# Optimization experiments

Hardware: AMD Instinct MI355X
Metric: run time of the kernel (lower is better)

## Reference

```python
import math
import jax, jax.numpy as jnp
import numpy as np

BATCH, DEPTH = 16, 12
N_NODES = 2 ** DEPTH - 1  # 4095, heap layout: children of i are 2i+1, 2i+2
IN_F, OUT_F, STATE_F = 512, 512, 256


def setup_inputs() -> dict:
    key = jax.random.key(0)
    ks = jax.random.split(key, 10)
    x_batch = jax.random.normal(ks[0], (BATCH, N_NODES, IN_F), dtype=jnp.float32)
    idx_batch = jnp.arange(BATCH, dtype=jnp.int32)
    W_in = jax.random.normal(ks[1], (IN_F, IN_F), dtype=jnp.float32) / math.sqrt(IN_F)
    b_in = jnp.zeros((IN_F,), dtype=jnp.float32)
    u1 = jax.random.uniform(ks[2], (STATE_F,), dtype=jnp.float32)
    u2 = jax.random.uniform(ks[3], (STATE_F,), dtype=jnp.float32)
    nu_log = jnp.log(-0.5 * jnp.log(u1 + 1e-6))
    theta_log = jnp.log(2.0 * math.pi * u2)
    lam_mod = jnp.exp(-jnp.exp(nu_log))
    gamma_log = jnp.log(jnp.sqrt(1.0 - jnp.square(lam_mod)))
    B_re = jax.random.normal(ks[4], (STATE_F, IN_F), dtype=jnp.float32) / math.sqrt(2 * IN_F)
    B_im = jax.random.normal(ks[5], (STATE_F, IN_F), dtype=jnp.float32) / math.sqrt(2 * IN_F)
    C_re = jax.random.normal(ks[6], (OUT_F, STATE_F), dtype=jnp.float32) / math.sqrt(STATE_F)
    C_im = jax.random.normal(ks[7], (OUT_F, STATE_F), dtype=jnp.float32) / math.sqrt(STATE_F)
    return dict(x_batch=x_batch, idx_batch=idx_batch, W_in=W_in, b_in=b_in,
                nu_log=nu_log, theta_log=theta_log, gamma_log=gamma_log,
                B_re=B_re, B_im=B_im, C_re=C_re, C_im=C_im)


def reference(x_batch, idx_batch, W_in, b_in, nu_log, theta_log, gamma_log,
              B_re, B_im, C_re, C_im):
    bsz, n_nodes, _ = x_batch.shape
    depth = int(round(math.log2(n_nodes + 1)))
    S = B_re.shape[0]

    # LRU constants (complex lambda kept as (re, im) pair)
    lam_mod = jnp.exp(-jnp.exp(nu_log))           # [S]
    th = jnp.exp(theta_log)
    lr, li = lam_mod * jnp.cos(th), lam_mod * jnp.sin(th)
    gamma = jnp.exp(gamma_log)                    # [S]

    proj = x_batch @ W_in.T + b_in                # [B, N, IN]
    # complex input term (proj is real): proj @ B^T
    in_re = jnp.einsum('bni,si->bns', proj, B_re) # [B, N, S]
    in_im = jnp.einsum('bni,si->bns', proj, B_im)

    h_re = jnp.zeros((bsz, n_nodes, S), dtype=proj.dtype)
    h_im = jnp.zeros((bsz, n_nodes, S), dtype=proj.dtype)

    # process levels bottom-up; level d nodes occupy [2^d-1, 2^{d+1}-1)
    for d in range(depth - 1, -1, -1):
        a, b = 2 ** d - 1, 2 ** (d + 1) - 1
        n = b - a
        if d == depth - 1:  # leaves: left/right = -1 -> zero child state
            cr = jnp.zeros((bsz, n, S), dtype=proj.dtype)
            ci = jnp.zeros((bsz, n, S), dtype=proj.dtype)
        else:
            # children of nodes [a, b) are the contiguous block [2a+1, 2b+1)
            cr = h_re[:, 2 * a + 1:2 * b + 1].reshape(bsz, n, 2, S).sum(axis=2)
            ci = h_im[:, 2 * a + 1:2 * b + 1].reshape(bsz, n, 2, S).sum(axis=2)
        hr = lr * cr - li * ci + gamma * in_re[:, a:b]
        hi = lr * ci + li * cr + gamma * in_im[:, a:b]
        h_re = h_re.at[:, a:b].set(hr)
        h_im = h_im.at[:, a:b].set(hi)

    # y = Re(h @ C^T), computed once on final states (same math as per-level scatter)
    outputs = jnp.einsum('bns,os->bno', h_re, C_re) - jnp.einsum('bns,os->bno', h_im, C_im)
    return outputs
```

## Files before the change

### kernel.cpp

```cpp
#include <hip/hip_runtime.h>


#define ROWS 65520
#define KDIM 512

typedef __attribute__((ext_vector_type(8))) short bf16x8;
typedef __attribute__((ext_vector_type(4))) float f32x4;

__device__ __forceinline__ unsigned short f2bf(float f) {
    unsigned int u = __float_as_uint(f);
    unsigned int r = (u + 0x7FFFu + ((u >> 16) & 1u)) >> 16;
    return (unsigned short)r;
}
__device__ __forceinline__ float b2f(unsigned short h) {
    return __uint_as_float(((unsigned int)h) << 16);
}
__device__ __forceinline__ float b2f_lo(unsigned int p) {
    return __uint_as_float(p << 16);
}
__device__ __forceinline__ float b2f_hi(unsigned int p) {
    return __uint_as_float(p & 0xFFFF0000u);
}

#define PC_BASE   1024
#define PB_BASE   2048
#define CVT_BASE  2176
#define CVT_BLKS  2048
#define PREP_GRID 4224
#define CVT_N4    8386560

__global__ __launch_bounds__(256) void prep_all(const float* __restrict__ x,
                                                unsigned short* __restrict__ x16,
                                                const float* __restrict__ W,
                                                const float* __restrict__ Bre,
                                                const float* __restrict__ Bim,
                                                const float* __restrict__ gamma_log,
                                                unsigned short* __restrict__ M16,
                                                const float* __restrict__ bin,
                                                float* __restrict__ biasc,
                                                const float* __restrict__ Cre,
                                                const float* __restrict__ Cim,
                                                unsigned short* __restrict__ C16) {
    __shared__ float Bs[16][17];
    __shared__ float Ws[16][17];
    const int blk = blockIdx.x;
    const int t = threadIdx.x;

    if (blk < PC_BASE) {
        const int bx = blk & 31;
        const int by = blk >> 5;
        const int tx = t & 15;
        const int ty = t >> 4;
        const int j  = bx * 16 + tx;
        const int cc = by * 16 + ty;
        const float* Bsel = (cc < 256) ? (Bre + (size_t)cc * 512)
                                       : (Bim + (size_t)(cc - 256) * 512);
        float acc = 0.f;
        for (int kt = 0; kt < 512; kt += 16) {
            Bs[ty][tx] = Bsel[kt + tx];
            Ws[ty][tx] = W[(size_t)(kt + ty) * 512 + j];
            __syncthreads();
#pragma unroll
            for (int k = 0; k < 16; ++k) acc += Bs[ty][k] * Ws[k][tx];
            __syncthreads();
        }
        float g = expf(gamma_log[cc & 255]);
        M16[(size_t)cc * 512 + j] = f2bf(acc * g);
    } else if (blk < PB_BASE) {
        int idx = (blk - PC_BASE) * 256 + t;
        int o = idx >> 9;
        int s = idx & 511;
        float v = (s < 256) ? Cre[(size_t)o * 256 + s] : -Cim[(size_t)o * 256 + (s - 256)];
        C16[idx] = f2bf(v);
    } else if (blk < CVT_BASE) {
        const int c = (blk - PB_BASE) * 4 + (t >> 6);
        const int lane = t & 63;
        const float* Bsel = (c < 256) ? (Bre + (size_t)c * 512)
                                      : (Bim + (size_t)(c - 256) * 512);
        float acc = 0.f;
#pragma unroll
        for (int i = lane; i < 512; i += 64) acc += bin[i] * Bsel[i];
#pragma unroll
        for (int off = 32; off > 0; off >>= 1) acc += __shfl_down(acc, off, 64);
        if (lane == 0) biasc[c] = acc * expf(gamma_log[c & 255]);
    } else {
        int i = (blk - CVT_BASE) * 256 + t;
#pragma unroll 4
        for (; i < CVT_N4; i += CVT_BLKS * 256) {
            float4 v = ((const float4*)x)[i];
            ushort4 o;
            o.x = f2bf(v.x); o.y = f2bf(v.y); o.z = f2bf(v.z); o.w = f2bf(v.w);
            ((ushort4*)x16)[i] = o;
        }
    }
}

template <bool OUT_BF16>
__global__ __launch_bounds__(256) void gemm_mfma(const unsigned short* __restrict__ A,
                                                 const unsigned short* __restrict__ Bm,
                                                 const float* __restrict__ bias,
                                                 void* __restrict__ Cout,
                                                 int Mrows) {
    __shared__ __align__(16) unsigned short As[2][128 * 64];
    __shared__ __align__(16) unsigned short Bs[2][128 * 64];
    const int t = threadIdx.x;
    const int lane = t & 63;
    const int w = t >> 6;
    const int wr = (w >> 1) * 64;
    const int wc = (w & 1) * 64;
    const int p = blockIdx.x;
    const int xcd = p & 7;
    const int q = p >> 3;
    const int colblk = q & 3;
    const int rg = q >> 2;
    const int col0 = colblk * 128;

    int arow[4], akoff[4], ldsoff[4];
    const unsigned short* gbB[4];
#pragma unroll
    for (int qq = 0; qq < 4; ++qq) {
        int c_   = qq * 256 + t;
        int row_ = c_ >> 3;
        int kc_  = c_ & 7;
        int kg_  = kc_ ^ (row_ & 7);
        arow[qq]  = row_;
        akoff[qq] = kg_ * 8;
        ldsoff[qq] = c_ * 8;
        gbB[qq] = Bm + (size_t)(col0 + row_) * KDIM + kg_ * 8;
    }
    const unsigned short* gaB[4];

#define SET_TILE_A(ROW0)                                                       \
    do {                                                                       \
        _Pragma("unroll")                                                      \
        for (int qq = 0; qq < 4; ++qq) {                                       \
            int ar_ = (ROW0) + arow[qq]; if (ar_ >= Mrows) ar_ = Mrows - 1;    \
            gaB[qq] = A + (size_t)ar_ * KDIM + akoff[qq];                      \
        }                                                                      \
    } while (0)

#define STAGE(pb, KT)                                                          \
    do {                                                                       \
        _Pragma("unroll")                                                      \
        for (int qq = 0; qq < 4; ++qq) {                                       \
            __builtin_amdgcn_global_load_lds(                                  \
                (const __attribute__((address_space(1))) unsigned int*)(gaB[qq] + (KT)), \
                (__attribute__((address_space(3))) unsigned int*)(&As[pb][ldsoff[qq]]), \
                16, 0, 0);                                                     \
            __builtin_amdgcn_global_load_lds(                                  \
                (const __attribute__((address_space(1))) unsigned int*)(gbB[qq] + (KT)), \
                (__attribute__((address_space(3))) unsigned int*)(&Bs[pb][ldsoff[qq]]), \
                16, 0, 0);                                                     \
        }                                                                      \
    } while (0)

    f32x4 acc[4][4] = {};

    int rowblk = xcd * 64 + rg * 4;
    int row0 = rowblk * 128;
    int kt0 = (rowblk & 7) * 64;
    SET_TILE_A(row0);
    STAGE(0, kt0);
    __syncthreads();

    int cur = 0;
    for (int j = 0; j < 4; ++j) {
        for (int it = 0; it < 8; ++it) {
            if (it < 7) {
                STAGE(cur ^ 1, (kt0 + (it + 1) * 64) & 511);
            } else if (j < 3) {
                const int nrowblk = rowblk + 1;
                SET_TILE_A(nrowblk * 128);
                STAGE(cur ^ 1, (nrowblk & 7) * 64);
            }
            __builtin_amdgcn_s_setprio(1);
#pragma unroll
            for (int kk = 0; kk < 64; kk += 32) {
                const int kgc = kk >> 3;
                bf16x8 af[4], bfr[4];
#pragma unroll
                for (int i = 0; i < 4; ++i) {
                    int row = wr + i * 16 + (lane & 15);
                    int kca = (kgc + (lane >> 4)) ^ (row & 7);
                    af[i] = *(const bf16x8*)(&As[cur][row * 64 + kca * 8]);
                    int colr = wc + i * 16 + (lane & 15);
                    int kcb = (kgc + (lane >> 4)) ^ (colr & 7);
                    bfr[i] = *(const bf16x8*)(&Bs[cur][colr * 64 + kcb * 8]);
                }
#pragma unroll
                for (int i = 0; i < 4; ++i)
#pragma unroll
                    for (int jj = 0; jj < 4; ++jj)
                        acc[i][jj] = __builtin_amdgcn_mfma_f32_16x16x32_bf16(
                            af[i], bfr[jj], acc[i][jj], 0, 0, 0);
            }
            __builtin_amdgcn_s_setprio(0);
            __syncthreads();
            cur ^= 1;
        }

        const int cq = lane >> 4;
        const int cl = lane & 15;
#pragma unroll
        for (int i = 0; i < 4; ++i) {
#pragma unroll
            for (int jj = 0; jj < 4; ++jj) {
#pragma unroll
                for (int r = 0; r < 4; ++r) {
                    int grow = row0 + wr + i * 16 + cq * 4 + r;
                    int gcol = col0 + wc + jj * 16 + cl;
                    if (grow < Mrows) {
                        float v = acc[i][jj][r];
                        if (bias) v += bias[gcol];
                        if (OUT_BF16)
                            ((unsigned short*)Cout)[(size_t)grow * 512 + gcol] = f2bf(v);
                        else
                            ((float*)Cout)[(size_t)grow * 512 + gcol] = v;
                    }
                    acc[i][jj][r] = 0.f;
                }
            }
        }

        rowblk += 1;
        row0 = rowblk * 128;
        kt0 = (rowblk & 7) * 64;
    }
#undef STAGE
#undef SET_TILE_A
}

template <int E>
__global__ __launch_bounds__(256) void tree_up2(unsigned short* __restrict__ buf,
                                                const float* __restrict__ nu_log,
                                                const float* __restrict__ theta_log,
                                                int root_base, int nroots) {
    const int b = blockIdx.x;
    const int h = threadIdx.x >> 7;
    const int j2 = (threadIdx.x & 127) * 2;
    const int rr = blockIdx.y * 2 + h;
    if (rr >= nroots) return;
    const int rs = root_base + rr;
    constexpr int LEAVES = 1 << E;
    constexpr int NODES = LEAVES - 1;

    float lr0, li0, lr1, li1;
    { const float lam = expf(-expf(nu_log[j2]));     const float th = expf(theta_log[j2]);
      lr0 = lam * cosf(th); li0 = lam * sinf(th); }
    { const float lam = expf(-expf(nu_log[j2 + 1])); const float th = expf(theta_log[j2 + 1]);
      lr1 = lam * cosf(th); li1 = lam * sinf(th); }
    const size_t base = (size_t)b * 4095;

    unsigned int pr[LEAVES], pi[LEAVES];
    const int nbL = ((rs + 1) << E) - 1;
#pragma unroll
    for (int i = 0; i < LEAVES; ++i) {
        const size_t r = (base + nbL + i) * 512;
        pr[i] = *(const unsigned int*)(buf + r + j2);
        pi[i] = *(const unsigned int*)(buf + r + 256 + j2);
    }
    unsigned int qr[NODES], qi[NODES];
#pragma unroll
    for (int e = E - 1; e >= 0; --e) {
#pragma unroll
        for (int i = 0; i < (1 << e); ++i) {
            const int idx = LEAVES - (2 << e) + i;
            const size_t r = (base + (((rs + 1) << e) - 1) + i) * 512;
            qr[idx] = *(const unsigned int*)(buf + r + j2);
            qi[idx] = *(const unsigned int*)(buf + r + 256 + j2);
        }
    }
    __builtin_amdgcn_sched_barrier(0);

    float vr0[LEAVES], vi0[LEAVES], vr1[LEAVES], vi1[LEAVES];
#pragma unroll
    for (int i = 0; i < LEAVES; ++i) {
        vr0[i] = b2f_lo(pr[i]); vr1[i] = b2f_hi(pr[i]);
        vi0[i] = b2f_lo(pi[i]); vi1[i] = b2f_hi(pi[i]);
    }
#pragma unroll
    for (int e = E - 1; e >= 0; --e) {
#pragma unroll
        for (int i = 0; i < (1 << e); ++i) {
            const int idx = LEAVES - (2 << e) + i;
            const float cr0 = vr0[2 * i] + vr0[2 * i + 1];
            const float ci0 = vi0[2 * i] + vi0[2 * i + 1];
            const float cr1 = vr1[2 * i] + vr1[2 * i + 1];
            const float ci1 = vi1[2 * i] + vi1[2 * i + 1];
            const float hr0 = lr0 * cr0 - li0 * ci0 + b2f_lo(qr[idx]);
            const float hi0 = lr0 * ci0 + li0 * cr0 + b2f_lo(qi[idx]);
            const float hr1 = lr1 * cr1 - li1 * ci1 + b2f_hi(qr[idx]);
            const float hi1 = lr1 * ci1 + li1 * cr1 + b2f_hi(qi[idx]);
            const size_t r = (base + (((rs + 1) << e) - 1) + i) * 512;
            *(unsigned int*)(buf + r + j2) =
                (unsigned int)f2bf(hr0) | ((unsigned int)f2bf(hr1) << 16);
            *(unsigned int*)(buf + r + 256 + j2) =
                (unsigned int)f2bf(hi0) | ((unsigned int)f2bf(hi1) << 16);
            vr0[i] = hr0; vi0[i] = hi0; vr1[i] = hr1; vi1[i] = hi1;
        }
    }
}

extern "C" void kernel_launch(void* const* d_in, const int* in_sizes, int n_in,
                              void* d_out, int out_size, void* d_ws, size_t ws_size,
                              hipStream_t stream) {
    const float* x         = (const float*)d_in[0];
    const float* W_in      = (const float*)d_in[2];
    const float* b_in      = (const float*)d_in[3];
    const float* nu_log    = (const float*)d_in[4];
    const float* theta_log = (const float*)d_in[5];
    const float* gamma_log = (const float*)d_in[6];
    const float* B_re      = (const float*)d_in[7];
    const float* B_im      = (const float*)d_in[8];
    const float* C_re      = (const float*)d_in[9];
    const float* C_im      = (const float*)d_in[10];
    float* out = (float*)d_out;

    char* ws = (char*)d_ws;
    const size_t HB = (size_t)ROWS * 512 * 2;
    unsigned short* x16   = (unsigned short*)ws;
    unsigned short* hb16  = (unsigned short*)(ws + HB);
    unsigned short* M16   = (unsigned short*)(ws + 2 * HB);
    unsigned short* C16   = (unsigned short*)(ws + 2 * HB + 512 * 512 * 2);
    float*          biasc = (float*)(ws + 2 * HB + 2 * 512 * 512 * 2);

    prep_all<<<PREP_GRID, 256, 0, stream>>>(x, x16, W_in, B_re, B_im, gamma_log,
                                            M16, b_in, biasc, C_re, C_im, C16);

    gemm_mfma<true><<<512, 256, 0, stream>>>(x16, M16, biasc, hb16, ROWS);

    tree_up2<4><<<dim3(16, 64), 256, 0, stream>>>(hb16, nu_log, theta_log, 127, 128);
    tree_up2<4><<<dim3(16, 4),  256, 0, stream>>>(hb16, nu_log, theta_log, 7, 8);
    tree_up2<3><<<dim3(16, 1),  256, 0, stream>>>(hb16, nu_log, theta_log, 0, 1);

    gemm_mfma<false><<<512, 256, 0, stream>>>(hb16, C16, nullptr, out, ROWS);
}
```

Baseline: 398.4 us.

## Halve GEMM K-tile to 32 with new LDS swizzle; batch fp32-to-bf16 conversion loads

The GEMM K-tile shrinks from 64 to 32, so LDS use per block halves and there are twice as many pipeline stages with a __syncthreads each. The XOR swizzle is replaced by a rotation swizzle suited to 4-chunk rows, and the starting K offset per row block now rotates over 16 positions. The x fp32-to-bf16 conversion issues all 16 strided loads before any store to get more memory parallelism, with a guarded fallback for the tail. Smaller LDS may raise occupancy, but the extra barriers and the shorter MFMA run per stage could reduce compute efficiency.

```diff
diff --git a/kernel.cpp b/kernel.cpp
--- a/kernel.cpp
+++ b/kernel.cpp
@@ -28,6 +28,7 @@
 #define CVT_BLKS  2048
 #define PREP_GRID 4224
 #define CVT_N4    8386560
+#define CVT_STR   (CVT_BLKS * 256)
 
 __global__ __launch_bounds__(256) void prep_all(const float* __restrict__ x,
                                                 unsigned short* __restrict__ x16,
@@ -84,13 +85,45 @@
         for (int off = 32; off > 0; off >>= 1) acc += __shfl_down(acc, off, 64);
         if (lane == 0) biasc[c] = acc * expf(gamma_log[c & 255]);
     } else {
-        int i = (blk - CVT_BASE) * 256 + t;
-#pragma unroll 4
-        for (; i < CVT_N4; i += CVT_BLKS * 256) {
-            float4 v = ((const float4*)x)[i];
-            ushort4 o;
-            o.x = f2bf(v.x); o.y = f2bf(v.y); o.z = f2bf(v.z); o.w = f2bf(v.w);
-            ((ushort4*)x16)[i] = o;
+        const int i = (blk - CVT_BASE) * 256 + t;
+        const float4* src = (const float4*)x;
+        ushort4* dst = (ushort4*)x16;
+        if (i < CVT_N4 - 15 * CVT_STR) {
+            float4 v0  = src[i];
+            float4 v1  = src[i +  1 * CVT_STR];
+            float4 v2  = src[i +  2 * CVT_STR];
+            float4 v3  = src[i +  3 * CVT_STR];
+            float4 v4  = src[i +  4 * CVT_STR];
+            float4 v5  = src[i +  5 * CVT_STR];
+            float4 v6  = src[i +  6 * CVT_STR];
+            float4 v7  = src[i +  7 * CVT_STR];
+            float4 v8  = src[i +  8 * CVT_STR];
+            float4 v9  = src[i +  9 * CVT_STR];
+            float4 v10 = src[i + 10 * CVT_STR];
+            float4 v11 = src[i + 11 * CVT_STR];
+            float4 v12 = src[i + 12 * CVT_STR];
+            float4 v13 = src[i + 13 * CVT_STR];
+            float4 v14 = src[i + 14 * CVT_STR];
+            float4 v15 = src[i + 15 * CVT_STR];
+#define CVT1(K, V)                                                             \
+            { ushort4 o; o.x = f2bf(V.x); o.y = f2bf(V.y);                     \
+              o.z = f2bf(V.z); o.w = f2bf(V.w); dst[i + (K) * CVT_STR] = o; }
+            CVT1(0, v0)  CVT1(1, v1)  CVT1(2, v2)  CVT1(3, v3)
+            CVT1(4, v4)  CVT1(5, v5)  CVT1(6, v6)  CVT1(7, v7)
+            CVT1(8, v8)  CVT1(9, v9)  CVT1(10, v10) CVT1(11, v11)
+            CVT1(12, v12) CVT1(13, v13) CVT1(14, v14) CVT1(15, v15)
+#undef CVT1
+        } else {
+#pragma unroll
+            for (int k = 0; k < 16; ++k) {
+                int idx = i + k * CVT_STR;
+                if (idx < CVT_N4) {
+                    float4 v = src[idx];
+                    ushort4 o;
+                    o.x = f2bf(v.x); o.y = f2bf(v.y); o.z = f2bf(v.z); o.w = f2bf(v.w);
+                    dst[idx] = o;
+                }
+            }
         }
     }
 }
@@ -101,8 +134,8 @@
                                                  const float* __restrict__ bias,
                                                  void* __restrict__ Cout,
                                                  int Mrows) {
-    __shared__ __align__(16) unsigned short As[2][128 * 64];
-    __shared__ __align__(16) unsigned short Bs[2][128 * 64];
+    __shared__ __align__(16) unsigned short As[2][128 * 32];
+    __shared__ __align__(16) unsigned short Bs[2][128 * 32];
     const int t = threadIdx.x;
     const int lane = t & 63;
     const int w = t >> 6;
@@ -115,25 +148,25 @@
     const int rg = q >> 2;
     const int col0 = colblk * 128;
 
-    int arow[4], akoff[4], ldsoff[4];
-    const unsigned short* gbB[4];
-#pragma unroll
-    for (int qq = 0; qq < 4; ++qq) {
+    int arow[2], akoff[2], ldsoff[2];
+    const unsigned short* gbB[2];
+#pragma unroll
+    for (int qq = 0; qq < 2; ++qq) {
         int c_   = qq * 256 + t;
-        int row_ = c_ >> 3;
-        int kc_  = c_ & 7;
-        int kg_  = kc_ ^ (row_ & 7);
+        int row_ = c_ >> 2;
+        int sl_  = c_ & 3;
+        int kc_  = (sl_ - (row_ >> 1)) & 3;
         arow[qq]  = row_;
-        akoff[qq] = kg_ * 8;
+        akoff[qq] = kc_ * 8;
         ldsoff[qq] = c_ * 8;
-        gbB[qq] = Bm + (size_t)(col0 + row_) * KDIM + kg_ * 8;
-    }
-    const unsigned short* gaB[4];
+        gbB[qq] = Bm + (size_t)(col0 + row_) * KDIM + kc_ * 8;
+    }
+    const unsigned short* gaB[2];
 
 #define SET_TILE_A(ROW0)                                                       \
     do {                                                                       \
         _Pragma("unroll")                                                      \
-        for (int qq = 0; qq < 4; ++qq) {                                       \
+        for (int qq = 0; qq < 2; ++qq) {                                       \
             int ar_ = (ROW0) + arow[qq]; if (ar_ >= Mrows) ar_ = Mrows - 1;    \
             gaB[qq] = A + (size_t)ar_ * KDIM + akoff[qq];                      \
         }                                                                      \
@@ -142,7 +175,7 @@
 #define STAGE(pb, KT)                                                          \
     do {                                                                       \
         _Pragma("unroll")                                                      \
-        for (int qq = 0; qq < 4; ++qq) {                                       \
+        for (int qq = 0; qq < 2; ++qq) {                                       \
             __builtin_amdgcn_global_load_lds(                                  \
                 (const __attribute__((address_space(1))) unsigned int*)(gaB[qq] + (KT)), \
                 (__attribute__((address_space(3))) unsigned int*)(&As[pb][ldsoff[qq]]), \
@@ -158,34 +191,32 @@
 
     int rowblk = xcd * 64 + rg * 4;
     int row0 = rowblk * 128;
-    int kt0 = (rowblk & 7) * 64;
+    int kt0 = (rowblk & 15) * 32;
     SET_TILE_A(row0);
     STAGE(0, kt0);
     __syncthreads();
 
     int cur = 0;
     for (int j = 0; j < 4; ++j) {
-        for (int it = 0; it < 8; ++it) {
-            if (it < 7) {
-                STAGE(cur ^ 1, (kt0 + (it + 1) * 64) & 511);
+        for (int it = 0; it < 16; ++it) {
+            if (it < 15) {
+                STAGE(cur ^ 1, (kt0 + (it + 1) * 32) & 511);
             } else if (j < 3) {
                 const int nrowblk = rowblk + 1;
                 SET_TILE_A(nrowblk * 128);
-                STAGE(cur ^ 1, (nrowblk & 7) * 64);
+                STAGE(cur ^ 1, (nrowblk & 15) * 32);
             }
             __builtin_amdgcn_s_setprio(1);
-#pragma unroll
-            for (int kk = 0; kk < 64; kk += 32) {
-                const int kgc = kk >> 3;
+            {
                 bf16x8 af[4], bfr[4];
 #pragma unroll
                 for (int i = 0; i < 4; ++i) {
                     int row = wr + i * 16 + (lane & 15);
-                    int kca = (kgc + (lane >> 4)) ^ (row & 7);
-                    af[i] = *(const bf16x8*)(&As[cur][row * 64 + kca * 8]);
+                    int sa  = ((lane >> 4) + (row >> 1)) & 3;
+                    af[i] = *(const bf16x8*)(&As[cur][row * 32 + sa * 8]);
                     int colr = wc + i * 16 + (lane & 15);
-                    int kcb = (kgc + (lane >> 4)) ^ (colr & 7);
-                    bfr[i] = *(const bf16x8*)(&Bs[cur][colr * 64 + kcb * 8]);
+                    int sb  = ((lane >> 4) + (colr >> 1)) & 3;
+                    bfr[i] = *(const bf16x8*)(&Bs[cur][colr * 32 + sb * 8]);
                 }
 #pragma unroll
                 for (int i = 0; i < 4; ++i)
@@ -224,7 +255,7 @@
 
         rowblk += 1;
         row0 = rowblk * 128;
-        kt0 = (rowblk & 7) * 64;
+        kt0 = (rowblk & 15) * 32;
     }
 #undef STAGE
 #undef SET_TILE_A
```

Result: slower. 413.4 us (+3.8%).

## Fuse fp32-to-bf16 input conversion into first GEMM's A-tile loading

Applied to the files above, without the earlier changes.

Removes the separate pass that converted x from fp32 to bf16 in the prep kernel. The first GEMM now reads fp32 A tiles into registers, starts the B async LDS load, runs the MFMA block, then converts and writes A to the other LDS buffer before the barrier. This avoids writing and re-reading a 64MB bf16 copy of x. In exchange, A staging goes through registers instead of direct global-to-LDS loads, which raises register pressure and VALU work inside the GEMM loop.

```diff
diff --git a/kernel.cpp b/kernel.cpp
--- a/kernel.cpp
+++ b/kernel.cpp
@@ -24,14 +24,9 @@
 
 #define PC_BASE   1024
 #define PB_BASE   2048
-#define CVT_BASE  2176
-#define CVT_BLKS  2048
-#define PREP_GRID 4224
-#define CVT_N4    8386560
-
-__global__ __launch_bounds__(256) void prep_all(const float* __restrict__ x,
-                                                unsigned short* __restrict__ x16,
-                                                const float* __restrict__ W,
+#define PREP_GRID 2176
+
+__global__ __launch_bounds__(256) void prep_all(const float* __restrict__ W,
                                                 const float* __restrict__ Bre,
                                                 const float* __restrict__ Bim,
                                                 const float* __restrict__ gamma_log,
@@ -72,7 +67,7 @@
         int s = idx & 511;
         float v = (s < 256) ? Cre[(size_t)o * 256 + s] : -Cim[(size_t)o * 256 + (s - 256)];
         C16[idx] = f2bf(v);
-    } else if (blk < CVT_BASE) {
+    } else {
         const int c = (blk - PB_BASE) * 4 + (t >> 6);
         const int lane = t & 63;
         const float* Bsel = (c < 256) ? (Bre + (size_t)c * 512)
@@ -83,26 +78,19 @@
 #pragma unroll
         for (int off = 32; off > 0; off >>= 1) acc += __shfl_down(acc, off, 64);
         if (lane == 0) biasc[c] = acc * expf(gamma_log[c & 255]);
-    } else {
-        int i = (blk - CVT_BASE) * 256 + t;
-#pragma unroll 4
-        for (; i < CVT_N4; i += CVT_BLKS * 256) {
-            float4 v = ((const float4*)x)[i];
-            ushort4 o;
-            o.x = f2bf(v.x); o.y = f2bf(v.y); o.z = f2bf(v.z); o.w = f2bf(v.w);
-            ((ushort4*)x16)[i] = o;
-        }
-    }
-}
-
-template <bool OUT_BF16>
-__global__ __launch_bounds__(256) void gemm_mfma(const unsigned short* __restrict__ A,
+    }
+}
+
+template <bool A_F32, bool OUT_BF16>
+__global__ __launch_bounds__(256) void gemm_mfma(const void* __restrict__ Ain,
                                                  const unsigned short* __restrict__ Bm,
                                                  const float* __restrict__ bias,
                                                  void* __restrict__ Cout,
                                                  int Mrows) {
     __shared__ __align__(16) unsigned short As[2][128 * 64];
     __shared__ __align__(16) unsigned short Bs[2][128 * 64];
+    const unsigned short* A16 = (const unsigned short*)Ain;
+    const float* A32 = (const float*)Ain;
     const int t = threadIdx.x;
     const int lane = t & 63;
     const int w = t >> 6;
@@ -128,29 +116,61 @@
         ldsoff[qq] = c_ * 8;
         gbB[qq] = Bm + (size_t)(col0 + row_) * KDIM + kg_ * 8;
     }
-    const unsigned short* gaB[4];
+    const unsigned short* ga16[4];
+    const float* ga32[4];
+    float4 fa[4][2];
 
 #define SET_TILE_A(ROW0)                                                       \
     do {                                                                       \
         _Pragma("unroll")                                                      \
         for (int qq = 0; qq < 4; ++qq) {                                       \
             int ar_ = (ROW0) + arow[qq]; if (ar_ >= Mrows) ar_ = Mrows - 1;    \
-            gaB[qq] = A + (size_t)ar_ * KDIM + akoff[qq];                      \
+            if constexpr (A_F32)                                               \
+                ga32[qq] = A32 + (size_t)ar_ * KDIM + akoff[qq];               \
+            else                                                               \
+                ga16[qq] = A16 + (size_t)ar_ * KDIM + akoff[qq];               \
         }                                                                      \
     } while (0)
 
-#define STAGE(pb, KT)                                                          \
-    do {                                                                       \
-        _Pragma("unroll")                                                      \
-        for (int qq = 0; qq < 4; ++qq) {                                       \
-            __builtin_amdgcn_global_load_lds(                                  \
-                (const __attribute__((address_space(1))) unsigned int*)(gaB[qq] + (KT)), \
-                (__attribute__((address_space(3))) unsigned int*)(&As[pb][ldsoff[qq]]), \
-                16, 0, 0);                                                     \
+#define STAGE_B(pb, KT)                                                        \
+    do {                                                                       \
+        _Pragma("unroll")                                                      \
+        for (int qq = 0; qq < 4; ++qq)                                         \
             __builtin_amdgcn_global_load_lds(                                  \
                 (const __attribute__((address_space(1))) unsigned int*)(gbB[qq] + (KT)), \
                 (__attribute__((address_space(3))) unsigned int*)(&Bs[pb][ldsoff[qq]]), \
                 16, 0, 0);                                                     \
+    } while (0)
+
+#define STAGE_A16(pb, KT)                                                      \
+    do {                                                                       \
+        _Pragma("unroll")                                                      \
+        for (int qq = 0; qq < 4; ++qq)                                         \
+            __builtin_amdgcn_global_load_lds(                                  \
+                (const __attribute__((address_space(1))) unsigned int*)(ga16[qq] + (KT)), \
+                (__attribute__((address_space(3))) unsigned int*)(&As[pb][ldsoff[qq]]), \
+                16, 0, 0);                                                     \
+    } while (0)
+
+#define LOAD_A32(KT)                                                           \
+    do {                                                                       \
+        _Pragma("unroll")                                                      \
+        for (int qq = 0; qq < 4; ++qq) {                                       \
+            fa[qq][0] = *(const float4*)(ga32[qq] + (KT));                     \
+            fa[qq][1] = *(const float4*)(ga32[qq] + (KT) + 4);                 \
+        }                                                                      \
+    } while (0)
+
+#define WRITE_A32(pb)                                                          \
+    do {                                                                       \
+        _Pragma("unroll")                                                      \
+        for (int qq = 0; qq < 4; ++qq) {                                       \
+            uint4 u;                                                           \
+            u.x = (unsigned int)f2bf(fa[qq][0].x) | ((unsigned int)f2bf(fa[qq][0].y) << 16); \
+            u.y = (unsigned int)f2bf(fa[qq][0].z) | ((unsigned int)f2bf(fa[qq][0].w) << 16); \
+            u.z = (unsigned int)f2bf(fa[qq][1].x) | ((unsigned int)f2bf(fa[qq][1].y) << 16); \
+            u.w = (unsigned int)f2bf(fa[qq][1].z) | ((unsigned int)f2bf(fa[qq][1].w) << 16); \
+            *(uint4*)(&As[pb][ldsoff[qq]]) = u;                                \
         }                                                                      \
     } while (0)
 
@@ -160,18 +180,37 @@
     int row0 = rowblk * 128;
     int kt0 = (rowblk & 7) * 64;
     SET_TILE_A(row0);
-    STAGE(0, kt0);
+    if constexpr (A_F32) {
+        LOAD_A32(kt0);
+        STAGE_B(0, kt0);
+        WRITE_A32(0);
+    } else {
+        STAGE_A16(0, kt0);
+        STAGE_B(0, kt0);
+    }
     __syncthreads();
 
     int cur = 0;
     for (int j = 0; j < 4; ++j) {
         for (int it = 0; it < 8; ++it) {
+            const bool st = (it < 7) || (j < 3);
+            int nkt = 0;
             if (it < 7) {
-                STAGE(cur ^ 1, (kt0 + (it + 1) * 64) & 511);
+                nkt = (kt0 + (it + 1) * 64) & 511;
             } else if (j < 3) {
                 const int nrowblk = rowblk + 1;
                 SET_TILE_A(nrowblk * 128);
-                STAGE(cur ^ 1, (nrowblk & 7) * 64);
+                nkt = (nrowblk & 7) * 64;
+            }
+            if (st) {
+                if constexpr (A_F32) {
+                    LOAD_A32(nkt);
+                    STAGE_B(cur ^ 1, nkt);
+                    __builtin_amdgcn_sched_barrier(0);
+                } else {
+                    STAGE_A16(cur ^ 1, nkt);
+                    STAGE_B(cur ^ 1, nkt);
+                }
             }
             __builtin_amdgcn_s_setprio(1);
 #pragma unroll
@@ -195,6 +234,9 @@
                             af[i], bfr[jj], acc[i][jj], 0, 0, 0);
             }
             __builtin_amdgcn_s_setprio(0);
+            if (st) {
+                if constexpr (A_F32) WRITE_A32(cur ^ 1);
+            }
             __syncthreads();
             cur ^= 1;
         }
@@ -226,7 +268,10 @@
         row0 = rowblk * 128;
         kt0 = (rowblk & 7) * 64;
     }
-#undef STAGE
+#undef WRITE_A32
+#undef LOAD_A32
+#undef STAGE_A16
+#undef STAGE_B
 #undef SET_TILE_A
 }
 
@@ -318,20 +363,19 @@
 
     char* ws = (char*)d_ws;
     const size_t HB = (size_t)ROWS * 512 * 2;
-    unsigned short* x16   = (unsigned short*)ws;
-    unsigned short* hb16  = (unsigned short*)(ws + HB);
-    unsigned short* M16   = (unsigned short*)(ws + 2 * HB);
-    unsigned short* C16   = (unsigned short*)(ws + 2 * HB + 512 * 512 * 2);
-    float*          biasc = (float*)(ws + 2 * HB + 2 * 512 * 512 * 2);
-
-    prep_all<<<PREP_GRID, 256, 0, stream>>>(x, x16, W_in, B_re, B_im, gamma_log,
+    unsigned short* hb16  = (unsigned short*)ws;
+    unsigned short* M16   = (unsigned short*)(ws + HB);
+    unsigned short* C16   = (unsigned short*)(ws + HB + 512 * 512 * 2);
+    float*          biasc = (float*)(ws + HB + 2 * 512 * 512 * 2);
+
+    prep_all<<<PREP_GRID, 256, 0, stream>>>(W_in, B_re, B_im, gamma_log,
                                             M16, b_in, biasc, C_re, C_im, C16);
 
-    gemm_mfma<true><<<512, 256, 0, stream>>>(x16, M16, biasc, hb16, ROWS);
+    gemm_mfma<true, true><<<512, 256, 0, stream>>>(x, M16, biasc, hb16, ROWS);
 
     tree_up2<4><<<dim3(16, 64), 256, 0, stream>>>(hb16, nu_log, theta_log, 127, 128);
     tree_up2<4><<<dim3(16, 4),  256, 0, stream>>>(hb16, nu_log, theta_log, 7, 8);
     tree_up2<3><<<dim3(16, 1),  256, 0, stream>>>(hb16, nu_log, theta_log, 0, 1);
 
-    gemm_mfma<false><<<512, 256, 0, stream>>>(hb16, C16, nullptr, out, ROWS);
-}
+    gemm_mfma<false, false><<<512, 256, 0, stream>>>(hb16, C16, nullptr, out, ROWS);
+}
```

After: 404.9 us. Within noise of the previous version (+1.6%).
